# Kernel tuning notes

Measured on AMD Instinct MI355X. Metric: run time of the kernel, lower is better.

The kernel has to match this reference:

```python
import jax, jax.numpy as jnp
import numpy as np

H, W = 64, 64
C = 256
NH = 8
WS = 8
SS = 4
N = WS * WS
HD = C // NH
HIDDEN = 4 * C
CPB_HIDDEN = 512
EPS = 1e-6


def _window_partition(x, ws):
    B, H_, W_, C_ = x.shape
    x = x.reshape(B, H_ // ws, ws, W_ // ws, ws, C_).transpose(0, 1, 3, 2, 4, 5)
    return x.reshape(-1, ws, ws, C_)


def _window_reverse(win, ws, H_, W_):
    B = win.shape[0] // ((H_ // ws) * (W_ // ws))
    x = win.reshape(B, H_ // ws, W_ // ws, ws, ws, -1).transpose(0, 1, 3, 2, 4, 5)
    return x.reshape(B, H_, W_, -1)


def _coords_table():
    # (1, 2*WS-1, 2*WS-1, 2) log-spaced continuous relative coords (SwinV2 CPB)
    ch = np.arange(-(WS - 1), WS)
    cw = np.arange(-(WS - 1), WS)
    t = np.stack(np.meshgrid(ch, cw, indexing='ij'), axis=-1)[None].astype(np.float32)
    t = t / (WS - 1) * 8.0
    t = np.sign(t) * np.log2(np.abs(t) + 1.0) / np.log2(8.0)
    return t.astype(np.float32)


def _rpe_index():
    coords = np.stack(np.meshgrid(np.arange(WS), np.arange(WS), indexing='ij'))
    cf = coords.reshape(2, -1)
    rel = (cf[:, :, None] - cf[:, None, :]).transpose(1, 2, 0)
    rel[:, :, 0] += WS - 1
    rel[:, :, 1] += WS - 1
    rel[:, :, 0] *= 2 * WS - 1
    return rel.sum(-1)  # (N, N) int


def _attn_mask():
    img = np.zeros((1, H, W, 1), np.float32)
    cnt = 0
    for hs in (slice(0, -WS), slice(-WS, -SS), slice(-SS, None)):
        for ws_ in (slice(0, -WS), slice(-WS, -SS), slice(-SS, None)):
            img[:, hs, ws_, :] = cnt
            cnt += 1
    mw = img.reshape(1, H // WS, WS, W // WS, WS, 1).transpose(0, 1, 3, 2, 4, 5).reshape(-1, N)
    am = mw[:, None, :] - mw[:, :, None]
    return np.where(am != 0, -100.0, 0.0).astype(np.float32)  # (nW, N, N)


_TABLE = jnp.asarray(_coords_table())
_RPE = jnp.asarray(_rpe_index().reshape(-1))
_AMASK = jnp.asarray(_attn_mask())


def setup_inputs() -> dict:
    key = jax.random.key(0)
    ks = jax.random.split(key, 12)
    s = 0.02
    return {
        'x': jax.random.normal(ks[0], (32, H * W, C), jnp.float32),
        'qkv_w': jax.random.normal(ks[1], (C, 3 * C), jnp.float32) * s,
        'q_bias': jnp.zeros((C,), jnp.float32),
        'v_bias': jnp.zeros((C,), jnp.float32),
        'logit_scale': jnp.log(10.0 * jnp.ones((NH, 1, 1), jnp.float32)),
        'cpb_w1': jax.random.normal(ks[2], (2, CPB_HIDDEN), jnp.float32) * s,
        'cpb_b1': jnp.zeros((CPB_HIDDEN,), jnp.float32),
        'cpb_w2': jax.random.normal(ks[3], (CPB_HIDDEN, NH), jnp.float32) * s,
        'proj_w': jax.random.normal(ks[4], (C, C), jnp.float32) * s,
        'proj_b': jnp.zeros((C,), jnp.float32),
        'norm1_scale': jnp.ones((C,), jnp.float32),
        'norm1_bias': jnp.zeros((C,), jnp.float32),
        'norm2_scale': jnp.ones((C,), jnp.float32),
        'norm2_bias': jnp.zeros((C,), jnp.float32),
        'fc1_w': jax.random.normal(ks[5], (C, HIDDEN), jnp.float32) * s,
        'fc1_b': jnp.zeros((HIDDEN,), jnp.float32),
        'fc2_w': jax.random.normal(ks[6], (HIDDEN, C), jnp.float32) * s,
        'fc2_b': jnp.zeros((C,), jnp.float32),
    }


def _layernorm(y, scale, bias):
    mu = jnp.mean(y, axis=-1, keepdims=True)
    var = jnp.mean(jnp.square(y - mu), axis=-1, keepdims=True)
    return (y - mu) * jax.lax.rsqrt(var + EPS) * scale + bias


def _l2n(t):
    return t * jax.lax.rsqrt(jnp.maximum(jnp.sum(t * t, axis=-1, keepdims=True), 1e-12))


def reference(x, qkv_w, q_bias, v_bias, logit_scale, cpb_w1, cpb_b1, cpb_w2,
              proj_w, proj_b, norm1_scale, norm1_bias, norm2_scale, norm2_bias,
              fc1_w, fc1_b, fc2_w, fc2_b):
    B, L, C_ = x.shape
    nW = _AMASK.shape[0]
    shortcut = x

    # cyclic shift + window partition
    xi = x.reshape(B, H, W, C_)
    xi = jnp.roll(xi, (-SS, -SS), axis=(1, 2))
    xw = _window_partition(xi, WS).reshape(-1, N, C_)  # (B_, N, C)
    B_ = xw.shape[0]

    # qkv with q/v bias only (k bias is zero)
    qkv_bias = jnp.concatenate([q_bias, jnp.zeros_like(v_bias), v_bias])
    qkv = xw @ qkv_w + qkv_bias
    qkv = qkv.reshape(B_, N, 3, NH, HD).transpose(2, 0, 3, 1, 4)
    q, k, v = qkv[0], qkv[1], qkv[2]  # (B_, NH, N, HD)

    # cosine attention with learned clamped logit scale
    attn = jnp.einsum('bhnd,bhmd->bhnm', _l2n(q), _l2n(k))
    scale = jnp.exp(jnp.minimum(logit_scale, np.log(100.0)))  # (NH,1,1)
    attn = attn * scale

    # continuous-position-bias MLP -> relative position bias, 16*sigmoid
    bias_table = jax.nn.relu(_TABLE @ cpb_w1 + cpb_b1) @ cpb_w2  # (1,2WS-1,2WS-1,NH)
    bias_table = bias_table.reshape(-1, NH)
    rpb = bias_table[_RPE].reshape(N, N, NH).transpose(2, 0, 1)  # (NH,N,N)
    attn = attn + (16.0 * jax.nn.sigmoid(rpb))[None]

    # shifted-window mask
    attn = attn.reshape(B_ // nW, nW, NH, N, N) + _AMASK[None, :, None]
    attn = jax.nn.softmax(attn.reshape(B_, NH, N, N), axis=-1)

    out = jnp.einsum('bhnm,bhmd->bnhd', attn, v).reshape(B_, N, C_)
    out = out @ proj_w + proj_b

    # window reverse + reverse cyclic shift
    out = _window_reverse(out.reshape(-1, WS, WS, C_), WS, H, W)
    out = jnp.roll(out, (SS, SS), axis=(1, 2)).reshape(B, L, C_)

    # SwinV2 post-norm residuals
    x1 = shortcut + _layernorm(out, norm1_scale, norm1_bias)
    h = jax.nn.gelu(x1 @ fc1_w + fc1_b) @ fc2_w + fc2_b
    return x1 + _layernorm(h, norm2_scale, norm2_bias)
```

## Files before the change

### kernel.cpp

```cpp
#include <hip/hip_runtime.h>

typedef __bf16 bf16;
typedef __bf16 bf16x8 __attribute__((ext_vector_type(8)));
typedef __bf16 bf16x4 __attribute__((ext_vector_type(4)));
typedef float  f32x4  __attribute__((ext_vector_type(4)));

#define MFMA16(a, b, c) __builtin_amdgcn_mfma_f32_16x16x32_bf16(a, b, c, 0, 0, 0)

__device__ __forceinline__ void gload_lds16(const void* g, void* l) {
    __builtin_amdgcn_global_load_lds((const __attribute__((address_space(1))) void*)g,
                                     (__attribute__((address_space(3))) void*)l, 16, 0, 0);
}

__device__ __forceinline__ long win2orig(long r) {
    long b = r >> 12; int rem = (int)(r & 4095);
    int widx = rem >> 6, t = rem & 63;
    int rp = ((widx >> 3) << 3) + (t >> 3), cp = ((widx & 7) << 3) + (t & 7);
    int rr = (rp + 4) & 63, cc = (cp + 4) & 63;
    return (b << 12) + rr * 64 + cc;
}

template <int GELU>
__global__ __launch_bounds__(256) void gemm_bt(const bf16* __restrict__ A,
                                               const bf16* __restrict__ Bt,
                                               const float* __restrict__ bias,
                                               bf16* __restrict__ C,
                                               int M, int N, int K) {
    __shared__ bf16 As[2][4096];
    __shared__ bf16 Bs[2][4096];
    const int t = threadIdx.x;
    const int w = t >> 6, l = t & 63;
    const int l15 = l & 15, q4 = l >> 4;
    const int wm = w >> 1, wn = w & 1;

    const unsigned gx = gridDim.x;
    const unsigned nwg = gx * gridDim.y;
    const unsigned id0 = blockIdx.y * gx + blockIdx.x;
    const unsigned swz = (id0 & 7u) * (nwg >> 3) + (id0 >> 3);
    const unsigned bx = swz % gx, by = swz / gx;

    const long row0 = (long)by * 128;
    const int col0 = (int)bx * 128;

    const bf16* aP = A + (row0 + w * 16 + l15) * (long)K + q4 * 8;
    const bf16* bP = Bt + (long)(col0 + w * 16 + l15) * K + q4 * 8;
    const long step64 = 64L * K;

    f32x4 acc[4][4];
#pragma unroll
    for (int i = 0; i < 4; i++)
#pragma unroll
        for (int j = 0; j < 4; j++)
#pragma unroll
            for (int r = 0; r < 4; r++) acc[i][j][r] = 0.f;

    const int KT = K >> 5;

    gload_lds16(aP,          &As[0][w * 512]);
    gload_lds16(aP + step64, &As[0][w * 512 + 2048]);
    gload_lds16(bP,          &Bs[0][w * 512]);
    gload_lds16(bP + step64, &Bs[0][w * 512 + 2048]);
    aP += 32; bP += 32;
    __syncthreads();

    int cur = 0;
    for (int kt = 0; kt < KT; ++kt) {
        if (kt + 1 < KT) {
            gload_lds16(aP,          &As[cur ^ 1][w * 512]);
            gload_lds16(aP + step64, &As[cur ^ 1][w * 512 + 2048]);
            gload_lds16(bP,          &Bs[cur ^ 1][w * 512]);
            gload_lds16(bP + step64, &Bs[cur ^ 1][w * 512 + 2048]);
            aP += 32; bP += 32;
        }
        bf16x8 af[4], bfv[4];
#pragma unroll
        for (int mi = 0; mi < 4; mi++) af[mi] = *(const bf16x8*)(&As[cur][(wm * 4 + mi) * 512 + l * 8]);
#pragma unroll
        for (int nj = 0; nj < 4; nj++) bfv[nj] = *(const bf16x8*)(&Bs[cur][(wn * 4 + nj) * 512 + l * 8]);
#pragma unroll
        for (int mi = 0; mi < 4; mi++)
#pragma unroll
            for (int nj = 0; nj < 4; nj++) acc[mi][nj] = MFMA16(af[mi], bfv[nj], acc[mi][nj]);
        __syncthreads();
        cur ^= 1;
    }

    float cb[4];
#pragma unroll
    for (int nj = 0; nj < 4; nj++) cb[nj] = bias[col0 + wn * 64 + nj * 16 + l15];

#pragma unroll
    for (int mi = 0; mi < 4; mi++) {
#pragma unroll
        for (int reg = 0; reg < 4; reg++) {
            long r = row0 + wm * 64 + mi * 16 + q4 * 4 + reg;
            bf16* cpn = C + r * (long)N + col0 + wn * 64 + l15;
#pragma unroll
            for (int nj = 0; nj < 4; nj++) {
                float v = acc[mi][nj][reg] + cb[nj];
                if (GELU) {
                    float v2 = v * v;
                    float tt = v * fmaf(v2, -0.10294702f, -2.30218094f);
                    float e = __builtin_amdgcn_exp2f(tt);
                    v = v * __builtin_amdgcn_rcpf(1.f + e);
                }
                cpn[nj * 16] = (bf16)v;
            }
        }
    }
}

__global__ __launch_bounds__(64) void attn_kernel(const bf16* __restrict__ qkv,
                                                  const float* __restrict__ bias16,
                                                  const float* __restrict__ logit_scale,
                                                  bf16* __restrict__ outp) {
    __shared__ bf16 P[64 * 72];
    __shared__ bf16 Vt[32 * 72];
    const int unit = blockIdx.x;
    const int w = unit >> 3, h = unit & 7;
    const int l = threadIdx.x;
    const int l15 = l & 15, q4 = l >> 4;
    const bf16* base = qkv + (long)w * 64 * 768;

    {
        const bf16* vp = base + l * 768 + 512 + h * 32;
#pragma unroll
        for (int c = 0; c < 4; c++) {
            bf16x8 vv = *(const bf16x8*)(vp + c * 8);
#pragma unroll
            for (int j = 0; j < 8; j++) Vt[(c * 8 + j) * 72 + l] = vv[j];
        }
    }

    const float scale = __expf(fminf(logit_scale[h], 4.605170186f));

    bf16x8 qf[4], kf[4];
#pragma unroll
    for (int mi = 0; mi < 4; mi++) {
        const bf16* p = base + (mi * 16 + l15) * 768 + h * 32 + q4 * 8;
        bf16x8 xv = *(const bf16x8*)p;
        float fv[8]; float ss = 0.f;
#pragma unroll
        for (int j = 0; j < 8; j++) { fv[j] = (float)xv[j]; ss += fv[j] * fv[j]; }
        ss += __shfl_xor(ss, 16); ss += __shfl_xor(ss, 32);
        float rs = rsqrtf(fmaxf(ss, 1e-12f));
#pragma unroll
        for (int j = 0; j < 8; j++) qf[mi][j] = (bf16)(fv[j] * rs);
    }
#pragma unroll
    for (int nj = 0; nj < 4; nj++) {
        const bf16* p = base + (nj * 16 + l15) * 768 + 256 + h * 32 + q4 * 8;
        bf16x8 xv = *(const bf16x8*)p;
        float fv[8]; float ss = 0.f;
#pragma unroll
        for (int j = 0; j < 8; j++) { fv[j] = (float)xv[j]; ss += fv[j] * fv[j]; }
        ss += __shfl_xor(ss, 16); ss += __shfl_xor(ss, 32);
        float rs = rsqrtf(fmaxf(ss, 1e-12f));
#pragma unroll
        for (int j = 0; j < 8; j++) kf[nj][j] = (bf16)(fv[j] * rs);
    }

    f32x4 acc[4][4];
#pragma unroll
    for (int i = 0; i < 4; i++)
#pragma unroll
        for (int j = 0; j < 4; j++)
#pragma unroll
            for (int r = 0; r < 4; r++) acc[i][j][r] = 0.f;
#pragma unroll
    for (int mi = 0; mi < 4; mi++)
#pragma unroll
        for (int nj = 0; nj < 4; nj++) acc[mi][nj] = MFMA16(qf[mi], kf[nj], acc[mi][nj]);

    const int widx = w & 63, wr = widx >> 3, wc = widx & 7;
    const bool edge = (wr == 7) || (wc == 7);
    int crid[4];
    if (edge) {
#pragma unroll
        for (int nj = 0; nj < 4; nj++) {
            int m = nj * 16 + l15;
            int R = wr * 8 + (m >> 3), Cc = wc * 8 + (m & 7);
            crid[nj] = ((R < 56) ? 0 : (R < 60 ? 1 : 2)) * 3 + ((Cc < 56) ? 0 : (Cc < 60 ? 1 : 2));
        }
    }
    const float* bh = bias16 + h * 4096;
#pragma unroll
    for (int mi = 0; mi < 4; mi++) {
#pragma unroll
        for (int reg = 0; reg < 4; reg++) {
            int n = mi * 16 + q4 * 4 + reg;
            const float* bp = bh + n * 64;
            int nrid = 0;
            if (edge) {
                int R = wr * 8 + (n >> 3), Cc = wc * 8 + (n & 7);
                nrid = ((R < 56) ? 0 : (R < 60 ? 1 : 2)) * 3 + ((Cc < 56) ? 0 : (Cc < 60 ? 1 : 2));
            }
#pragma unroll
            for (int nj = 0; nj < 4; nj++) {
                float v = acc[mi][nj][reg] * scale + bp[nj * 16 + l15];
                if (edge && nrid != crid[nj]) v -= 100.f;
                acc[mi][nj][reg] = v;
            }
        }
    }

#pragma unroll
    for (int mi = 0; mi < 4; mi++) {
#pragma unroll
        for (int reg = 0; reg < 4; reg++) {
            float mx = fmaxf(fmaxf(acc[mi][0][reg], acc[mi][1][reg]),
                             fmaxf(acc[mi][2][reg], acc[mi][3][reg]));
            mx = fmaxf(mx, __shfl_xor(mx, 1));
            mx = fmaxf(mx, __shfl_xor(mx, 2));
            mx = fmaxf(mx, __shfl_xor(mx, 4));
            mx = fmaxf(mx, __shfl_xor(mx, 8));
            float s = 0.f;
#pragma unroll
            for (int nj = 0; nj < 4; nj++) {
                float e = __expf(acc[mi][nj][reg] - mx);
                acc[mi][nj][reg] = e; s += e;
            }
            s += __shfl_xor(s, 1); s += __shfl_xor(s, 2);
            s += __shfl_xor(s, 4); s += __shfl_xor(s, 8);
            float inv = 1.f / s;
            int n = mi * 16 + q4 * 4 + reg;
#pragma unroll
            for (int nj = 0; nj < 4; nj++)
                P[n * 72 + nj * 16 + l15] = (bf16)(acc[mi][nj][reg] * inv);
        }
    }
    __syncthreads();

    f32x4 o[4][2];
#pragma unroll
    for (int i = 0; i < 4; i++)
#pragma unroll
        for (int j = 0; j < 2; j++)
#pragma unroll
            for (int r = 0; r < 4; r++) o[i][j][r] = 0.f;
#pragma unroll
    for (int ks = 0; ks < 2; ks++) {
        bf16x8 vf[2];
#pragma unroll
        for (int nj = 0; nj < 2; nj++) vf[nj] = *(const bf16x8*)(&Vt[(nj * 16 + l15) * 72 + ks * 32 + q4 * 8]);
#pragma unroll
        for (int mi = 0; mi < 4; mi++) {
            bf16x8 pf = *(const bf16x8*)(&P[(mi * 16 + l15) * 72 + ks * 32 + q4 * 8]);
#pragma unroll
            for (int nj = 0; nj < 2; nj++) o[mi][nj] = MFMA16(pf, vf[nj], o[mi][nj]);
        }
    }

    bf16* op = outp + (long)w * 64 * 256 + h * 32;
#pragma unroll
    for (int mi = 0; mi < 4; mi++)
#pragma unroll
        for (int reg = 0; reg < 4; reg++) {
            int tok = mi * 16 + q4 * 4 + reg;
#pragma unroll
            for (int nj = 0; nj < 2; nj++)
                op[tok * 256 + nj * 16 + l15] = (bf16)o[mi][nj][reg];
        }
}

__global__ __launch_bounds__(256) void norm1_kernel(const bf16* __restrict__ pin,
                                                    const float* __restrict__ x,
                                                    const float* __restrict__ g,
                                                    const float* __restrict__ bb,
                                                    bf16* __restrict__ x1h) {
    const int tid = threadIdx.x;
    const int wid = tid >> 6, l = tid & 63;
    const long rl = (long)blockIdx.x * 4 + wid;
    bf16x4 v4 = *(const bf16x4*)(pin + rl * 256 + l * 4);
    float v[4]; float s = 0.f, sq = 0.f;
#pragma unroll
    for (int c = 0; c < 4; c++) { v[c] = (float)v4[c]; s += v[c]; sq += v[c] * v[c]; }
#pragma unroll
    for (int off = 1; off < 64; off <<= 1) { s += __shfl_xor(s, off); sq += __shfl_xor(sq, off); }
    float mu = s * 0.00390625f;
    float var = sq * 0.00390625f - mu * mu;
    float rstd = rsqrtf(var + 1e-6f);
    long orig = win2orig(rl);
    float4 xv = *(const float4*)(x + orig * 256 + l * 4);
    float4 gv = *(const float4*)(g + l * 4);
    float4 bv = *(const float4*)(bb + l * 4);
    bf16x4 oh;
    oh[0] = (bf16)(xv.x + ((v[0] - mu) * rstd * gv.x + bv.x));
    oh[1] = (bf16)(xv.y + ((v[1] - mu) * rstd * gv.y + bv.y));
    oh[2] = (bf16)(xv.z + ((v[2] - mu) * rstd * gv.z + bv.z));
    oh[3] = (bf16)(xv.w + ((v[3] - mu) * rstd * gv.w + bv.w));
    *(bf16x4*)(x1h + orig * 256 + l * 4) = oh;
}

__global__ __launch_bounds__(256) void norm2_kernel(const bf16* __restrict__ hin,
                                                    const bf16* __restrict__ x1h,
                                                    const float* __restrict__ g,
                                                    const float* __restrict__ bb,
                                                    float* __restrict__ outp) {
    const int tid = threadIdx.x;
    const int wid = tid >> 6, l = tid & 63;
    const long rl = (long)blockIdx.x * 4 + wid;
    bf16x4 v4 = *(const bf16x4*)(hin + rl * 256 + l * 4);
    float v[4]; float s = 0.f, sq = 0.f;
#pragma unroll
    for (int c = 0; c < 4; c++) { v[c] = (float)v4[c]; s += v[c]; sq += v[c] * v[c]; }
#pragma unroll
    for (int off = 1; off < 64; off <<= 1) { s += __shfl_xor(s, off); sq += __shfl_xor(sq, off); }
    float mu = s * 0.00390625f;
    float var = sq * 0.00390625f - mu * mu;
    float rstd = rsqrtf(var + 1e-6f);
    bf16x4 xv4 = *(const bf16x4*)(x1h + rl * 256 + l * 4);
    float4 gv = *(const float4*)(g + l * 4);
    float4 bv = *(const float4*)(bb + l * 4);
    float4 ov;
    ov.x = (float)xv4[0] + ((v[0] - mu) * rstd * gv.x + bv.x);
    ov.y = (float)xv4[1] + ((v[1] - mu) * rstd * gv.y + bv.y);
    ov.z = (float)xv4[2] + ((v[2] - mu) * rstd * gv.z + bv.z);
    ov.w = (float)xv4[3] + ((v[3] - mu) * rstd * gv.w + bv.w);
    *(float4*)(outp + rl * 256 + l * 4) = ov;
}

__global__ __launch_bounds__(256) void gather_cast(const float* __restrict__ x,
                                                   bf16* __restrict__ out) {
    const int tid = threadIdx.x;
    const int wid = tid >> 6, l = tid & 63;
    const long rl = (long)blockIdx.x * 4 + wid;
    long orig = win2orig(rl);
    float4 v = *(const float4*)(x + orig * 256 + l * 4);
    bf16x4 o = {(bf16)v.x, (bf16)v.y, (bf16)v.z, (bf16)v.w};
    *(bf16x4*)(out + rl * 256 + l * 4) = o;
}

__global__ void transpose_cast(const float* __restrict__ in, bf16* __restrict__ out, int K, int N) {
    int id = blockIdx.x * 256 + threadIdx.x;
    if (id < K * N) {
        int n = id / K, k = id - n * K;
        out[id] = (bf16)in[k * N + n];
    }
}

__global__ void build_qkv_bias(const float* __restrict__ qb, const float* __restrict__ vb,
                               float* __restrict__ out) {
    int i = blockIdx.x * 256 + threadIdx.x;
    if (i < 768) out[i] = (i < 256) ? qb[i] : ((i < 512) ? 0.f : vb[i - 512]);
}

__device__ __forceinline__ float cpcoord(int d) {
    float v = (float)d * (8.0f / 7.0f);
    float r = log2f(fabsf(v) + 1.0f) * (1.0f / 3.0f);
    return v < 0.f ? -r : r;
}

__global__ void cpb1(const float* __restrict__ w1, const float* __restrict__ b1,
                     const float* __restrict__ w2, float* __restrict__ tbl) {
    int a = threadIdx.x;
    if (a >= 225) return;
    int i = a / 15, j = a - i * 15;
    float t0 = cpcoord(i - 7), t1 = cpcoord(j - 7);
    float acc[8];
#pragma unroll
    for (int o = 0; o < 8; o++) acc[o] = 0.f;
    for (int jj = 0; jj < 512; jj++) {
        float hv = fmaf(t0, w1[jj], fmaf(t1, w1[512 + jj], b1[jj]));
        hv = fmaxf(hv, 0.f);
#pragma unroll
        for (int o = 0; o < 8; o++) acc[o] = fmaf(hv, w2[jj * 8 + o], acc[o]);
    }
#pragma unroll
    for (int o = 0; o < 8; o++) tbl[a * 8 + o] = acc[o];
}

__global__ void cpb2(const float* __restrict__ tbl, float* __restrict__ bias16) {
    int id = blockIdx.x * 256 + threadIdx.x;
    if (id >= 32768) return;
    int h = id >> 12, n = (id >> 6) & 63, m = id & 63;
    int r0 = (n >> 3) - (m >> 3) + 7;
    int r1 = (n & 7) - (m & 7) + 7;
    float v = tbl[(r0 * 15 + r1) * 8 + h];
    bias16[id] = 16.f / (1.f + __expf(-v));
}

extern "C" void kernel_launch(void* const* d_in, const int* in_sizes, int n_in,
                              void* d_out, int out_size, void* d_ws, size_t ws_size,
                              hipStream_t stream) {
    const float* x   = (const float*)d_in[0];
    const float* qkvw= (const float*)d_in[1];
    const float* qb  = (const float*)d_in[2];
    const float* vb  = (const float*)d_in[3];
    const float* ls  = (const float*)d_in[4];
    const float* cw1 = (const float*)d_in[5];
    const float* cb1 = (const float*)d_in[6];
    const float* cw2 = (const float*)d_in[7];
    const float* pw  = (const float*)d_in[8];
    const float* pb  = (const float*)d_in[9];
    const float* n1s = (const float*)d_in[10];
    const float* n1b = (const float*)d_in[11];
    const float* n2s = (const float*)d_in[12];
    const float* n2b = (const float*)d_in[13];
    const float* f1w = (const float*)d_in[14];
    const float* f1b = (const float*)d_in[15];
    const float* f2w = (const float*)d_in[16];
    const float* f2b = (const float*)d_in[17];

    char* ws = (char*)d_ws;
    if (ws_size < 471859200UL) return;
    bf16*  qkvBt   = (bf16*)(ws + 0);
    bf16*  projBt  = (bf16*)(ws + 393216);
    bf16*  fc1Bt   = (bf16*)(ws + 524288);
    bf16*  fc2Bt   = (bf16*)(ws + 1048576);
    float* qkvBias = (float*)(ws + 1572864);
    float* cpbTbl  = (float*)(ws + 1575936);
    float* bias16  = (float*)(ws + 1583360);
    bf16* xbf     = (bf16*)(ws + 2097152);
    bf16* qkvBuf  = (bf16*)(ws + 69206016);
    bf16* attnOut = (bf16*)(ws + 270532608);
    bf16* projOut = (bf16*)(ws + 337641472);
    bf16* x1h     = (bf16*)(ws + 404750336);
    bf16* hBuf    = (bf16*)(ws + 2097152);
    bf16* fc2Out  = (bf16*)(ws + 337641472);

    transpose_cast<<<768, 256, 0, stream>>>(qkvw, qkvBt, 256, 768);
    transpose_cast<<<256, 256, 0, stream>>>(pw, projBt, 256, 256);
    transpose_cast<<<1024, 256, 0, stream>>>(f1w, fc1Bt, 256, 1024);
    transpose_cast<<<1024, 256, 0, stream>>>(f2w, fc2Bt, 1024, 256);
    build_qkv_bias<<<3, 256, 0, stream>>>(qb, vb, qkvBias);
    cpb1<<<1, 256, 0, stream>>>(cw1, cb1, cw2, cpbTbl);
    cpb2<<<128, 256, 0, stream>>>(cpbTbl, bias16);

    gather_cast<<<32768, 256, 0, stream>>>(x, xbf);
    gemm_bt<0><<<dim3(6, 1024), 256, 0, stream>>>(xbf, qkvBt, qkvBias, qkvBuf, 131072, 768, 256);
    attn_kernel<<<16384, 64, 0, stream>>>(qkvBuf, bias16, ls, attnOut);
    gemm_bt<0><<<dim3(2, 1024), 256, 0, stream>>>(attnOut, projBt, pb, projOut, 131072, 256, 256);
    norm1_kernel<<<32768, 256, 0, stream>>>(projOut, x, n1s, n1b, x1h);
    gemm_bt<1><<<dim3(8, 1024), 256, 0, stream>>>(x1h, fc1Bt, f1b, hBuf, 131072, 1024, 256);
    gemm_bt<0><<<dim3(2, 1024), 256, 0, stream>>>(hBuf, fc2Bt, f2b, fc2Out, 131072, 256, 1024);
    norm2_kernel<<<32768, 256, 0, stream>>>(fc2Out, x1h, n2s, n2b, (float*)d_out);
}
```

Measured before the change: 1.039 ms.

## Enlarge GEMM tile to 256x256 and load MFMA fragments directly into registers

Replaces the LDS double-buffered 128x128 GEMM with a 512-thread kernel computing 256x256 tiles, where each wave loads its A/B fragments straight from global memory into registers with a two-stage register pipeline. This removes LDS staging and most block-wide syncs, and increases per-wave compute reuse. In exchange, operands are re-read by multiple waves through cache, global loads are less coalesced, and register pressure rises sharply, risking spills or low occupancy.

Result: slower. 1.187 ms (+14.2%).

```diff
diff --git a/kernel.cpp b/kernel.cpp
--- a/kernel.cpp
+++ b/kernel.cpp
@@ -6,11 +6,6 @@
 typedef float  f32x4  __attribute__((ext_vector_type(4)));
 
 #define MFMA16(a, b, c) __builtin_amdgcn_mfma_f32_16x16x32_bf16(a, b, c, 0, 0, 0)
-
-__device__ __forceinline__ void gload_lds16(const void* g, void* l) {
-    __builtin_amdgcn_global_load_lds((const __attribute__((address_space(1))) void*)g,
-                                     (__attribute__((address_space(3))) void*)l, 16, 0, 0);
-}
 
 __device__ __forceinline__ long win2orig(long r) {
     long b = r >> 12; int rem = (int)(r & 4095);
@@ -21,17 +16,15 @@
 }
 
 template <int GELU>
-__global__ __launch_bounds__(256) void gemm_bt(const bf16* __restrict__ A,
-                                               const bf16* __restrict__ Bt,
-                                               const float* __restrict__ bias,
-                                               bf16* __restrict__ C,
-                                               int M, int N, int K) {
-    __shared__ bf16 As[2][4096];
-    __shared__ bf16 Bs[2][4096];
+__global__ __launch_bounds__(512, 2) void gemm_bt(const bf16* __restrict__ A,
+                                                  const bf16* __restrict__ Bt,
+                                                  const float* __restrict__ bias,
+                                                  bf16* __restrict__ C,
+                                                  int M, int N, int K) {
     const int t = threadIdx.x;
     const int w = t >> 6, l = t & 63;
     const int l15 = l & 15, q4 = l >> 4;
-    const int wm = w >> 1, wn = w & 1;
+    const int wm = w >> 2, wn = w & 3;
 
     const unsigned gx = gridDim.x;
     const unsigned nwg = gx * gridDim.y;
@@ -39,61 +32,68 @@
     const unsigned swz = (id0 & 7u) * (nwg >> 3) + (id0 >> 3);
     const unsigned bx = swz % gx, by = swz / gx;
 
-    const long row0 = (long)by * 128;
-    const int col0 = (int)bx * 128;
-
-    const bf16* aP = A + (row0 + w * 16 + l15) * (long)K + q4 * 8;
-    const bf16* bP = Bt + (long)(col0 + w * 16 + l15) * K + q4 * 8;
-    const long step64 = 64L * K;
-
-    f32x4 acc[4][4];
-#pragma unroll
-    for (int i = 0; i < 4; i++)
+    const long row0 = (long)by * 256;
+    const int col0 = (int)bx * 256;
+
+    const long lK = (long)K;
+    const bf16* aBase = A + (row0 + wm * 128 + l15) * lK + q4 * 8;
+    const bf16* bBase = Bt + ((long)col0 + wn * 64 + l15) * lK + q4 * 8;
+    const long a16 = 16L * K;
+
+#define LOADA(dst, ss)                                                         \
+    do {                                                                       \
+        _Pragma("unroll")                                                      \
+        for (int mi = 0; mi < 8; mi++)                                         \
+            dst[mi] = *(const bf16x8*)(aBase + mi * a16 + (ss) * 32);          \
+    } while (0)
+#define LOADB(dst, ss)                                                         \
+    do {                                                                       \
+        _Pragma("unroll")                                                      \
+        for (int nj = 0; nj < 4; nj++)                                         \
+            dst[nj] = *(const bf16x8*)(bBase + nj * a16 + (ss) * 32);          \
+    } while (0)
+#define MFMA_ALL(af, bfv)                                                      \
+    do {                                                                       \
+        _Pragma("unroll")                                                      \
+        for (int mi = 0; mi < 8; mi++)                                         \
+            _Pragma("unroll")                                                  \
+            for (int nj = 0; nj < 4; nj++)                                     \
+                acc[mi][nj] = MFMA16(af[mi], bfv[nj], acc[mi][nj]);            \
+    } while (0)
+
+    f32x4 acc[8][4];
+#pragma unroll
+    for (int i = 0; i < 8; i++)
 #pragma unroll
         for (int j = 0; j < 4; j++)
 #pragma unroll
             for (int r = 0; r < 4; r++) acc[i][j][r] = 0.f;
 
-    const int KT = K >> 5;
-
-    gload_lds16(aP,          &As[0][w * 512]);
-    gload_lds16(aP + step64, &As[0][w * 512 + 2048]);
-    gload_lds16(bP,          &Bs[0][w * 512]);
-    gload_lds16(bP + step64, &Bs[0][w * 512 + 2048]);
-    aP += 32; bP += 32;
-    __syncthreads();
-
-    int cur = 0;
-    for (int kt = 0; kt < KT; ++kt) {
-        if (kt + 1 < KT) {
-            gload_lds16(aP,          &As[cur ^ 1][w * 512]);
-            gload_lds16(aP + step64, &As[cur ^ 1][w * 512 + 2048]);
-            gload_lds16(bP,          &Bs[cur ^ 1][w * 512]);
-            gload_lds16(bP + step64, &Bs[cur ^ 1][w * 512 + 2048]);
-            aP += 32; bP += 32;
-        }
-        bf16x8 af[4], bfv[4];
-#pragma unroll
-        for (int mi = 0; mi < 4; mi++) af[mi] = *(const bf16x8*)(&As[cur][(wm * 4 + mi) * 512 + l * 8]);
-#pragma unroll
-        for (int nj = 0; nj < 4; nj++) bfv[nj] = *(const bf16x8*)(&Bs[cur][(wn * 4 + nj) * 512 + l * 8]);
-#pragma unroll
-        for (int mi = 0; mi < 4; mi++)
-#pragma unroll
-            for (int nj = 0; nj < 4; nj++) acc[mi][nj] = MFMA16(af[mi], bfv[nj], acc[mi][nj]);
-        __syncthreads();
-        cur ^= 1;
-    }
+    const int S = K >> 5;
+
+    bf16x8 a0[8], b0[4], a1[8], b1[4];
+    LOADA(a0, 0); LOADB(b0, 0);
+
+    for (int s = 0; s + 2 <= S; s += 2) {
+        LOADA(a1, s + 1); LOADB(b1, s + 1);
+        MFMA_ALL(a0, b0);
+        if (s + 2 < S) { LOADA(a0, s + 2); LOADB(b0, s + 2); }
+        MFMA_ALL(a1, b1);
+        __builtin_amdgcn_s_barrier();
+    }
+#undef LOADA
+#undef LOADB
+#undef MFMA_ALL
 
     float cb[4];
 #pragma unroll
     for (int nj = 0; nj < 4; nj++) cb[nj] = bias[col0 + wn * 64 + nj * 16 + l15];
 
 #pragma unroll
-    for (int mi = 0; mi < 4; mi++) {
+    for (int mi = 0; mi < 8; mi++) {
 #pragma unroll
         for (int reg = 0; reg < 4; reg++) {
-            long r = row0 + wm * 64 + mi * 16 + q4 * 4 + reg;
+            long r = row0 + wm * 128 + mi * 16 + q4 * 4 + reg;
             bf16* cpn = C + r * (long)N + col0 + wn * 64 + l15;
 #pragma unroll
             for (int nj = 0; nj < 4; nj++) {
@@ -428,11 +428,11 @@
     cpb2<<<128, 256, 0, stream>>>(cpbTbl, bias16);
 
     gather_cast<<<32768, 256, 0, stream>>>(x, xbf);
-    gemm_bt<0><<<dim3(6, 1024), 256, 0, stream>>>(xbf, qkvBt, qkvBias, qkvBuf, 131072, 768, 256);
+    gemm_bt<0><<<dim3(3, 512), 512, 0, stream>>>(xbf, qkvBt, qkvBias, qkvBuf, 131072, 768, 256);
     attn_kernel<<<16384, 64, 0, stream>>>(qkvBuf, bias16, ls, attnOut);
-    gemm_bt<0><<<dim3(2, 1024), 256, 0, stream>>>(attnOut, projBt, pb, projOut, 131072, 256, 256);
+    gemm_bt<0><<<dim3(1, 512), 512, 0, stream>>>(attnOut, projBt, pb, projOut, 131072, 256, 256);
     norm1_kernel<<<32768, 256, 0, stream>>>(projOut, x, n1s, n1b, x1h);
-    gemm_bt<1><<<dim3(8, 1024), 256, 0, stream>>>(x1h, fc1Bt, f1b, hBuf, 131072, 1024, 256);
-    gemm_bt<0><<<dim3(2, 1024), 256, 0, stream>>>(hBuf, fc2Bt, f2b, fc2Out, 131072, 256, 1024);
+    gemm_bt<1><<<dim3(4, 512), 512, 0, stream>>>(x1h, fc1Bt, f1b, hBuf, 131072, 1024, 256);
+    gemm_bt<0><<<dim3(1, 512), 512, 0, stream>>>(hBuf, fc2Bt, f2b, fc2Out, 131072, 256, 1024);
     norm2_kernel<<<32768, 256, 0, stream>>>(fc2Out, x1h, n2s, n2b, (float*)d_out);
 }
```
